# Performance work log

Measured on AMD Instinct MI355X. Metric: run time of the kernel, lower is better.

Reference implementation:

```python
import jax, jax.numpy as jnp
import numpy as np

# Dimensions (ModelNet40-style point-cloud classification)
B, N, KNN, T = 4, 1024, 20, 10
BETA, LAM, EPS = 1.0, 1.0, 1e-6
TAU, TH_POS, TH_NEG = 20.0, 1.0, -1.0
NUM_CLASSES = 40


@jax.custom_vjp
def spike(x):
    # Heaviside with fast-sigmoid surrogate gradient (standard SNN practice)
    return (x >= 0).astype(x.dtype)

def _spike_fwd(x):
    return (x >= 0).astype(x.dtype), x

def _spike_bwd(x, g):
    return (g / (1.0 + jnp.abs(x)) ** 2,)

spike.defvjp(_spike_fwd, _spike_bwd)


def setup_inputs() -> dict:
    key = jax.random.key(0)
    ks = jax.random.split(key, 8)

    def lin(k, fin, fout):
        return jax.random.normal(k, (fin, fout), jnp.float32) / float(np.sqrt(fin))

    def cheb(k, fin, fout):  # [K=3, F_in, F_out] Chebyshev filter bank
        return jax.random.normal(k, (3, fin, fout), jnp.float32) / float(np.sqrt(fin))

    return {
        "point_cloud": jax.random.normal(ks[0], (B, N, 3), jnp.float32),
        "enc_W": lin(ks[1], 3, 64), "enc_b": jnp.zeros((64,), jnp.float32),
        "W0": cheb(ks[2], 64, 64), "b0": jnp.zeros((64,), jnp.float32),
        "W1": cheb(ks[3], 128, 128), "b1": jnp.zeros((128,), jnp.float32),
        "W2": cheb(ks[4], 256, 256), "b2": jnp.zeros((256,), jnp.float32),
        "ro_W": lin(ks[5], 512, NUM_CLASSES), "ro_b": jnp.zeros((NUM_CLASSES,), jnp.float32),
    }


def build_graph(pc):
    # Local-density-adaptive kNN graph: [B,N,KNN] neighbor idx, edge weights, per-node scale
    d2 = jnp.sum((pc[:, :, None, :] - pc[:, None, :, :]) ** 2, -1)  # [B,N,N]
    d2 = d2 + jnp.eye(pc.shape[1], dtype=pc.dtype) * 1e9            # exclude self
    negv, idx = jax.lax.top_k(-d2, KNN)
    dist = jnp.sqrt(jnp.maximum(-negv, 1e-12))                      # [B,N,KNN]
    sigma = BETA * jnp.mean(dist, -1) + EPS                         # adaptive sigma [B,N]
    w = jnp.exp(-dist ** 2 / sigma[..., None] ** 2)
    w = w / (jnp.sum(w, -1, keepdims=True) + EPS)                   # row-normalized
    return idx, w, LAM * sigma                                      # s_local = lambda*sigma


def lap_apply(x, idx, w, s):
    # Node-adaptive scaled Laplacian: s_i * (x_i - sum_j w_ij x_j); x: [B,T,N,F]
    neigh = jax.vmap(lambda xb, ib: xb[:, ib])(x, idx)              # [B,T,N,KNN,F]
    agg = jnp.einsum('bnk,btnkf->btnf', w, neigh)
    return s[:, None, :, None] * (x - agg)


def wavelet_conv(x, idx, w, s, Wc, bc):
    # Chebyshev order-3 graph wavelet conv: T0=x, T1=Lx, T2=2L(T1)-T0
    t1 = lap_apply(x, idx, w, s)
    t2 = 2.0 * lap_apply(t1, idx, w, s) - x
    return jnp.einsum('kbtnf,kfg->btng', jnp.stack([x, t1, t2]), Wc) + bc


def bipolar_lif(x):
    # Bipolar LIF with dual thresholds; soft reset; output concat([pos, neg]) doubles F
    decay = jnp.exp(jnp.asarray(-1.0 / TAU, x.dtype))
    def step(v, xt):
        v = decay * v + xt
        sp = spike(v - TH_POS)
        sn = spike(TH_NEG - v)
        v = v - sp * TH_POS - sn * TH_NEG
        return v, jnp.concatenate([sp, sn], -1)
    v0 = jnp.zeros((x.shape[0],) + x.shape[2:], x.dtype)
    _, out = jax.lax.scan(step, v0, jnp.swapaxes(x, 0, 1))          # scan over T
    return jnp.swapaxes(out, 0, 1)                                  # [B,T,N,2F]


def reference(point_cloud, enc_W, enc_b, W0, b0, W1, b1, W2, b2, ro_W, ro_b):
    idx, w, s = build_graph(point_cloud)
    feat = jax.nn.relu(point_cloud @ enc_W + enc_b)                 # [B,N,64]
    rates = jnp.clip(feat, 0.0, 1.0)
    u = jax.random.uniform(jax.random.key(42), (feat.shape[0], T) + feat.shape[1:], feat.dtype)
    spikes = (u < rates[:, None]).astype(feat.dtype)                # Poisson rate encoding [B,T,N,64]
    for Wc, bc in ((W0, b0), (W1, b1), (W2, b2)):
        spikes = bipolar_lif(wavelet_conv(spikes, idx, w, s, Wc, bc))
    rate = jnp.mean(spikes, axis=1)                                 # rate readout over time
    pooled = jnp.mean(rate, axis=1)                                 # global average pool over nodes
    return pooled @ ro_W + ro_b                                     # [B, NUM_CLASSES]
```

## Files before the change

### kernel.cpp

```cpp
#include <hip/hip_runtime.h>
#include <stdint.h>
#include <math.h>

#pragma clang fp contract(off)

#define NB 4
#define NN 1024
#define KNN 20
#define NT 10

__global__ __launch_bounds__(256) void graph_kernel(const float* __restrict__ pc,
        int* __restrict__ idx_out, float* __restrict__ w_out, float* __restrict__ s_out){
  int row = blockIdx.x;
  int b = row >> 10, i = row & (NN-1);
  int tid = threadIdx.x;
  __shared__ float d2s[NN];
  __shared__ unsigned long long red[256];
  __shared__ int   sel_idx[KNN];
  __shared__ float sel_d2[KNN];
  const float* pb = pc + (size_t)b*NN*3;
  float xi = pb[i*3+0], yi = pb[i*3+1], zi = pb[i*3+2];
  for (int j=tid; j<NN; j+=256){
    float dx = xi - pb[j*3+0];
    float dy = yi - pb[j*3+1];
    float dz = zi - pb[j*3+2];
    float d2 = dx*dx;
    d2 = d2 + dy*dy;
    d2 = d2 + dz*dz;
    if (j==i) d2 = d2 + 1e9f;
    d2s[j] = d2;
  }
  __syncthreads();
  for (int k=0;k<KNN;k++){
    unsigned long long best = 0xffffffffffffffffull;
    for (int j=tid;j<NN;j+=256){
      unsigned long long key = ((unsigned long long)__float_as_uint(d2s[j])<<32) | (unsigned int)j;
      if (key < best) best = key;
    }
    red[tid] = best;
    __syncthreads();
    for (int off=128; off>0; off>>=1){
      if (tid < off){ if (red[tid+off] < red[tid]) red[tid] = red[tid+off]; }
      __syncthreads();
    }
    if (tid==0){
      unsigned long long bk = red[0];
      int bj = (int)(bk & 0xffffffffu);
      sel_idx[k] = bj;
      sel_d2[k]  = __uint_as_float((unsigned int)(bk >> 32));
      d2s[bj] = __uint_as_float(0x7f800000u);
    }
    __syncthreads();
  }
  if (tid==0){
    float dist[KNN]; float dsum = 0.0f;
    for (int k=0;k<KNN;k++){ dist[k] = sqrtf(fmaxf(sel_d2[k], 1e-12f)); dsum = dsum + dist[k]; }
    float sigma = dsum / 20.0f;
    sigma = 1.0f * sigma + 1e-6f;
    float s2 = sigma * sigma;
    float wv[KNN]; float wsum = 0.0f;
    for (int k=0;k<KNN;k++){
      float ds = dist[k]*dist[k];
      wv[k] = expf((-ds)/s2);
      wsum = wsum + wv[k];
    }
    float denom = wsum + 1e-6f;
    for (int k=0;k<KNN;k++){
      w_out[(size_t)row*KNN+k]  = wv[k] / denom;
      idx_out[(size_t)row*KNN+k] = sel_idx[k];
    }
    s_out[row] = 1.0f * sigma;
  }
}

__global__ void enc_kernel(const float* __restrict__ pc, const float* __restrict__ W,
                           const float* __restrict__ bias, float* __restrict__ rates){
  int id = blockIdx.x*blockDim.x + threadIdx.x;
  if (id >= NB*NN*64) return;
  int f = id & 63; int bn = id >> 6;
  float p0 = pc[bn*3+0], p1 = pc[bn*3+1], p2 = pc[bn*3+2];
  float acc = fmaf(p0, W[0*64+f], 0.0f);
  acc = fmaf(p1, W[1*64+f], acc);
  acc = fmaf(p2, W[2*64+f], acc);
  acc = acc + bias[f];
  acc = fmaxf(acc, 0.0f);
  acc = fminf(fmaxf(acc, 0.0f), 1.0f);
  rates[id] = acc;
}

__device__ __forceinline__ uint32_t rotl32(uint32_t x, uint32_t r){ return (x<<r) | (x>>(32u-r)); }

__global__ void poisson_kernel(const float* __restrict__ rates, uint8_t* __restrict__ out){
  const uint32_t H = (uint32_t)(NB*NT*NN*64) / 2u;
  uint32_t i = blockIdx.x*blockDim.x + threadIdx.x;
  if (i >= H) return;
  const uint32_t ks0 = 0u, ks1 = 42u;
  const uint32_t ks2 = ks0 ^ ks1 ^ 0x1BD11BDAu;
  uint32_t x0 = i + ks0;
  uint32_t x1 = (i + H) + ks1;
#define TF4(a,b,c,d) \
  x0 += x1; x1 = rotl32(x1,a); x1 ^= x0; \
  x0 += x1; x1 = rotl32(x1,b); x1 ^= x0; \
  x0 += x1; x1 = rotl32(x1,c); x1 ^= x0; \
  x0 += x1; x1 = rotl32(x1,d); x1 ^= x0;
  TF4(13u,15u,26u,6u)  x0 += ks1; x1 += ks2 + 1u;
  TF4(17u,29u,16u,24u) x0 += ks2; x1 += ks0 + 2u;
  TF4(13u,15u,26u,6u)  x0 += ks0; x1 += ks1 + 3u;
  TF4(17u,29u,16u,24u) x0 += ks1; x1 += ks2 + 4u;
  TF4(13u,15u,26u,6u)  x0 += ks2; x1 += ks0 + 5u;
#undef TF4
  {
    uint32_t m = i;
    float u = __uint_as_float((x0 >> 9) | 0x3f800000u) - 1.0f;
    uint32_t f = m & 63u, n = (m >> 6) & (NN-1);
    uint32_t bt = m >> 16; uint32_t b = bt / NT;
    float rate = rates[(((size_t)b<<10) + n)*64 + f];
    out[m] = (u < rate) ? (uint8_t)1 : (uint8_t)0;
  }
  {
    uint32_t m = i + H;
    float u = __uint_as_float((x1 >> 9) | 0x3f800000u) - 1.0f;
    uint32_t f = m & 63u, n = (m >> 6) & (NN-1);
    uint32_t bt = m >> 16; uint32_t b = bt / NT;
    float rate = rates[(((size_t)b<<10) + n)*64 + f];
    out[m] = (u < rate) ? (uint8_t)1 : (uint8_t)0;
  }
}

__global__ void lap1_all_kernel(const uint8_t* __restrict__ x, const int* __restrict__ idx,
        const float* __restrict__ w, const float* __restrict__ s,
        float* __restrict__ t1, int t0, int F){
  int blk = blockIdx.x; int f = threadIdx.x;
  int bn = blk % (NB*NN); int tt = blk / (NB*NN);
  int b = bn >> 10; int n = bn & (NN-1); int t = t0 + tt;
  __shared__ int nidx[KNN]; __shared__ float nw[KNN]; __shared__ float sv;
  if (f < KNN){ nidx[f] = idx[(size_t)bn*KNN+f]; nw[f] = w[(size_t)bn*KNN+f]; }
  if (f == 0) sv = s[bn];
  __syncthreads();
  const uint8_t* xb = x + ((size_t)(b*NT + t)*NN)*F;
  float acc = 0.0f;
  for (int k=0;k<KNN;k++)
    acc = fmaf(nw[k], (float)xb[(size_t)nidx[k]*F + f], acc);
  float xv = (float)xb[(size_t)n*F + f];
  t1[((size_t)tt*(NB*NN) + bn)*F + f] = sv * (xv - acc);
}

__global__ void lap2_all_kernel(const uint8_t* __restrict__ x, const float* __restrict__ t1,
        const int* __restrict__ idx, const float* __restrict__ w, const float* __restrict__ s,
        float* __restrict__ t2, int t0, int F){
  int blk = blockIdx.x; int f = threadIdx.x;
  int bn = blk % (NB*NN); int tt = blk / (NB*NN);
  int b = bn >> 10; int n = bn & (NN-1); int t = t0 + tt;
  __shared__ int nidx[KNN]; __shared__ float nw[KNN]; __shared__ float sv;
  if (f < KNN){ nidx[f] = idx[(size_t)bn*KNN+f]; nw[f] = w[(size_t)bn*KNN+f]; }
  if (f == 0) sv = s[bn];
  __syncthreads();
  const float* t1b = t1 + ((size_t)tt*(NB*NN) + (size_t)b*NN)*F;
  float acc = 0.0f;
  for (int k=0;k<KNN;k++)
    acc = fmaf(nw[k], t1b[(size_t)nidx[k]*F + f], acc);
  float tv = t1[((size_t)tt*(NB*NN) + bn)*F + f];
  float lapv = sv * (tv - acc);
  const uint8_t* xb = x + ((size_t)(b*NT + t)*NN)*F;
  float xv = (float)xb[(size_t)n*F + f];
  t2[((size_t)tt*(NB*NN) + bn)*F + f] = 2.0f * lapv - xv;
}

template<int F, int G, int BN, int TN>
__global__ __launch_bounds__(256) void conv_gemm_kernel(const uint8_t* __restrict__ x,
        const float* __restrict__ t1, const float* __restrict__ t2,
        const float* __restrict__ W, float* __restrict__ abuf, int t0){
  constexpr int BM = 64, BK = 16, TM = 4;
  constexpr int NTX = BN / TN;
  constexpr int LDA = BM + 4;
  constexpr int LDB = BN + 4;
  __shared__ float As[BK * LDA];
  __shared__ float Ws[BK * LDB];

  const int tid = threadIdx.x;
  const int tx = tid % NTX, ty = tid / NTX;
  const int row0 = blockIdx.x * BM;
  const int g0 = blockIdx.y * BN;

  const int arow = tid >> 2;
  const int akg  = (tid & 3) * 4;
  const int grow = row0 + arow;
  const int tt_a = grow / (NB*NN);
  const int bn_a = grow % (NB*NN);
  const int b_a = bn_a >> 10, n_a = bn_a & (NN-1);
  const uint8_t* xrow  = x  + ((size_t)(b_a*NT + t0 + tt_a)*NN + n_a)*F;
  const float*   t1row = t1 + (size_t)grow * F;
  const float*   t2row = t2 + (size_t)grow * F;

  float acc[TM][TN];
  #pragma unroll
  for (int r=0;r<TM;r++)
    #pragma unroll
    for (int c=0;c<TN;c++) acc[r][c] = 0.0f;

  for (int s = 0; s < 3; ++s){
    for (int f0 = 0; f0 < F; f0 += BK){
      if (s == 0){
        uchar4 u = *(const uchar4*)(xrow + f0 + akg);
        As[(akg+0)*LDA + arow] = (float)u.x;
        As[(akg+1)*LDA + arow] = (float)u.y;
        As[(akg+2)*LDA + arow] = (float)u.z;
        As[(akg+3)*LDA + arow] = (float)u.w;
      } else {
        const float* src = ((s==1) ? t1row : t2row) + f0 + akg;
        float4 v = *(const float4*)src;
        As[(akg+0)*LDA + arow] = v.x;
        As[(akg+1)*LDA + arow] = v.y;
        As[(akg+2)*LDA + arow] = v.z;
        As[(akg+3)*LDA + arow] = v.w;
      }
      const float* Wsrc = W + ((size_t)(s*F + f0))*G + g0;
      #pragma unroll
      for (int e = 0; e < (BK*BN)/(256*4); ++e){
        int idx = tid + e*256;
        int wk = idx / (BN/4);
        int wg = (idx % (BN/4))*4;
        *(float4*)&Ws[wk*LDB + wg] = *(const float4*)(Wsrc + (size_t)wk*G + wg);
      }
      __syncthreads();
      #pragma unroll
      for (int k = 0; k < BK; ++k){
        float a[TM];
        *(float4*)a = *(const float4*)&As[k*LDA + ty*TM];
        float wv[TN];
        #pragma unroll
        for (int c = 0; c < TN; c += 4)
          *(float4*)&wv[c] = *(const float4*)&Ws[k*LDB + tx*TN + c];
        #pragma unroll
        for (int r=0;r<TM;r++)
          #pragma unroll
          for (int c=0;c<TN;c++)
            acc[r][c] = fmaf(a[r], wv[c], acc[r][c]);
      }
      __syncthreads();
    }
  }
  #pragma unroll
  for (int r=0;r<TM;r++){
    float* dst = abuf + (size_t)(row0 + ty*TM + r)*G + g0 + tx*TN;
    #pragma unroll
    for (int c=0;c<TN;c+=4)
      *(float4*)(dst + c) = *(float4*)&acc[r][c];
  }
}

__global__ void lif_kernel(const float* __restrict__ abuf, const float* __restrict__ bias,
        float* __restrict__ vbuf, uint8_t* __restrict__ out, int t0, int tc, int G, float decay){
  int id = blockIdx.x*blockDim.x + threadIdx.x;
  if (id >= NB*NN*G) return;
  int g = id % G;
  int bn = id / G;
  int b = bn >> 10, n = bn & (NN-1);
  float v = (t0 == 0) ? 0.0f : vbuf[id];
  float bg = bias[g];
  for (int tt=0; tt<tc; ++tt){
    float a = abuf[((size_t)tt*(NB*NN) + bn)*G + g] + bg;
    float vn = decay * v + a;
    float sp  = ((vn - 1.0f) >= 0.0f) ? 1.0f : 0.0f;
    float snk = ((-1.0f - vn) >= 0.0f) ? 1.0f : 0.0f;
    vn = vn - sp * 1.0f;
    vn = vn - snk * (-1.0f);
    v = vn;
    uint8_t* ob = out + ((size_t)(b*NT + t0 + tt)*NN + n)*((size_t)2*G);
    ob[g]   = (uint8_t)sp;
    ob[G+g] = (uint8_t)snk;
  }
  if (t0 + tc < NT) vbuf[id] = v;
}

__global__ void pool_partial_kernel(const uint8_t* __restrict__ sp, uint32_t* __restrict__ partial){
  int b = blockIdx.x >> 6;
  int chunk = blockIdx.x & 63;
  int n0 = chunk * 16;
  int u = threadIdx.x;
  uint32_t c0=0,c1=0,c2=0,c3=0;
  for (int t=0;t<NT;t++){
    for (int n=0;n<16;n++){
      const uint32_t* rowp = (const uint32_t*)(sp + ((size_t)(b*NT+t)*NN + n0+n)*512);
      uint32_t wv = rowp[u];
      c0 += wv & 0xffu;
      c1 += (wv >> 8) & 0xffu;
      c2 += (wv >> 16) & 0xffu;
      c3 += wv >> 24;
    }
  }
  uint32_t* op = partial + (size_t)blockIdx.x*512 + u*4;
  op[0]=c0; op[1]=c1; op[2]=c2; op[3]=c3;
}

__global__ __launch_bounds__(512) void finalize_head_kernel(const uint32_t* __restrict__ partial,
        const float* __restrict__ roW, const float* __restrict__ rob, float* __restrict__ out){
  int b = blockIdx.x;
  int f = threadIdx.x;
  __shared__ float pooled[512];
  uint32_t cnt = 0;
  for (int ch=0; ch<64; ch++)
    cnt += partial[((size_t)(b*64+ch))*512 + f];
  pooled[f] = (float)cnt / 10.0f / 1024.0f;
  __syncthreads();
  if (f < 40){
    float acc = 0.0f;
    for (int k=0;k<512;k++)
      acc = fmaf(pooled[k], roW[k*40+f], acc);
    out[b*40 + f] = acc + rob[f];
  }
}

extern "C" void kernel_launch(void* const* d_in, const int* in_sizes, int n_in,
                              void* d_out, int out_size, void* d_ws, size_t ws_size,
                              hipStream_t stream) {
  const float* pc   = (const float*)d_in[0];
  const float* encW = (const float*)d_in[1];
  const float* encB = (const float*)d_in[2];
  const float* W0   = (const float*)d_in[3];
  const float* b0   = (const float*)d_in[4];
  const float* W1   = (const float*)d_in[5];
  const float* b1   = (const float*)d_in[6];
  const float* W2   = (const float*)d_in[7];
  const float* b2   = (const float*)d_in[8];
  const float* roW  = (const float*)d_in[9];
  const float* rob  = (const float*)d_in[10];
  float* outp = (float*)d_out;

  char* p = (char*)d_ws;
  auto alloc = [&](size_t bytes)->char*{
    char* r = p; p += (bytes + 255) & ~(size_t)255; return r;
  };
  int*      idxb   = (int*)     alloc((size_t)NB*NN*KNN*4);
  float*    wb     = (float*)   alloc((size_t)NB*NN*KNN*4);
  float*    sb     = (float*)   alloc((size_t)NB*NN*4);
  float*    rates  = (float*)   alloc((size_t)NB*NN*64*4);
  float*    vbuf   = (float*)   alloc((size_t)NB*NN*256*4);
  uint32_t* partial= (uint32_t*)alloc((size_t)NB*64*512*4);
  uint8_t*  bufA   = (uint8_t*) alloc((size_t)NB*NT*NN*512);
  uint8_t*  bufB   = (uint8_t*) alloc((size_t)NB*NT*NN*512);

  size_t used = (size_t)(p - (char*)d_ws);
  size_t per_t = (size_t)NB*NN*256*4*3;
  int TC = 1;
  if (ws_size > used + per_t){
    size_t tcc = (ws_size - used) / per_t;
    TC = (tcc >= NT) ? NT : (int)tcc;
    if (TC < 1) TC = 1;
  }
  float* t1b  = (float*)alloc((size_t)NB*(size_t)TC*NN*256*4);
  float* t2b  = (float*)alloc((size_t)NB*(size_t)TC*NN*256*4);
  float* abuf = (float*)alloc((size_t)NB*(size_t)TC*NN*256*4);

  graph_kernel<<<NB*NN, 256, 0, stream>>>(pc, idxb, wb, sb);
  enc_kernel<<<(NB*NN*64 + 255)/256, 256, 0, stream>>>(pc, encW, encB, rates);
  {
    const uint32_t H = (uint32_t)(NB*NT*NN*64) / 2u;
    poisson_kernel<<<(H + 255)/256, 256, 0, stream>>>(rates, bufA);
  }

  float decay = expf(-1.0f / 20.0f);

  uint8_t* xin  = bufA;
  uint8_t* xout = bufB;
  for (int l=0; l<3; l++){
    int F = (l==0)?64:(l==1)?128:256;
    int G = F;
    const float* Wc = (l==0)?W0:(l==1)?W1:W2;
    const float* bc = (l==0)?b0:(l==1)?b1:b2;
    for (int t0=0; t0<NT; t0+=TC){
      int tc = (NT - t0 < TC) ? (NT - t0) : TC;
      int M = NB*NN*tc;
      lap1_all_kernel<<<NB*NN*tc, F, 0, stream>>>(xin, idxb, wb, sb, t1b, t0, F);
      lap2_all_kernel<<<NB*NN*tc, F, 0, stream>>>(xin, t1b, idxb, wb, sb, t2b, t0, F);
      if (l==0){
        dim3 grid(M/64, 1);
        conv_gemm_kernel<64,64,64,4><<<grid, 256, 0, stream>>>(xin, t1b, t2b, Wc, abuf, t0);
      } else if (l==1){
        dim3 grid(M/64, 2);
        conv_gemm_kernel<128,128,64,4><<<grid, 256, 0, stream>>>(xin, t1b, t2b, Wc, abuf, t0);
      } else {
        dim3 grid(M/64, 2);
        conv_gemm_kernel<256,256,128,8><<<grid, 256, 0, stream>>>(xin, t1b, t2b, Wc, abuf, t0);
      }
      lif_kernel<<<(NB*NN*G + 255)/256, 256, 0, stream>>>(abuf, bc, vbuf, xout, t0, tc, G, decay);
    }
    uint8_t* tmp = xin; xin = xout; xout = tmp;
  }

  pool_partial_kernel<<<NB*64, 128, 0, stream>>>(xin, partial);
  finalize_head_kernel<<<NB, 512, 0, stream>>>(partial, roW, rob, outp);
}
```

Measured before the change: 549.3 us.

## Pack multiple rows per Laplacian block and enlarge GEMM tiles to 128 rows

The Laplacian kernels are templated on F and now process 256/F rows per 256-thread block, so the small 64- and 128-wide layers no longer launch one tiny block per row. The conv GEMM tile grows from 64 to 128 rows with 8 rows per thread. Each thread's rows and columns are split into two halves to keep shared-memory reads conflict-free, and layer 1 now uses a single 128-wide column tile. This raises arithmetic intensity and per-thread reuse but increases register pressure and reduces the number of GEMM blocks.

```diff
diff --git a/kernel.cpp b/kernel.cpp
--- a/kernel.cpp
+++ b/kernel.cpp
@@ -127,51 +127,68 @@
   }
 }
 
-__global__ void lap1_all_kernel(const uint8_t* __restrict__ x, const int* __restrict__ idx,
-        const float* __restrict__ w, const float* __restrict__ s,
-        float* __restrict__ t1, int t0, int F){
-  int blk = blockIdx.x; int f = threadIdx.x;
-  int bn = blk % (NB*NN); int tt = blk / (NB*NN);
+template<int F>
+__global__ __launch_bounds__(256) void lap1_kernel2(const uint8_t* __restrict__ x,
+        const int* __restrict__ idx, const float* __restrict__ w, const float* __restrict__ s,
+        float* __restrict__ t1, int t0){
+  constexpr int R = 256 / F;
+  int tid = threadIdx.x;
+  int rsub = tid / F;
+  int f = tid % F;
+  int row = blockIdx.x * R + rsub;
+  int bn = row % (NB*NN); int tt = row / (NB*NN);
   int b = bn >> 10; int n = bn & (NN-1); int t = t0 + tt;
-  __shared__ int nidx[KNN]; __shared__ float nw[KNN]; __shared__ float sv;
-  if (f < KNN){ nidx[f] = idx[(size_t)bn*KNN+f]; nw[f] = w[(size_t)bn*KNN+f]; }
-  if (f == 0) sv = s[bn];
+  __shared__ int   nidx[R][KNN];
+  __shared__ float nw[R][KNN];
+  __shared__ float sv[R];
+  if (f < KNN){ nidx[rsub][f] = idx[(size_t)bn*KNN+f]; nw[rsub][f] = w[(size_t)bn*KNN+f]; }
+  if (f == 0) sv[rsub] = s[bn];
   __syncthreads();
   const uint8_t* xb = x + ((size_t)(b*NT + t)*NN)*F;
   float acc = 0.0f;
   for (int k=0;k<KNN;k++)
-    acc = fmaf(nw[k], (float)xb[(size_t)nidx[k]*F + f], acc);
+    acc = fmaf(nw[rsub][k], (float)xb[(size_t)nidx[rsub][k]*F + f], acc);
   float xv = (float)xb[(size_t)n*F + f];
-  t1[((size_t)tt*(NB*NN) + bn)*F + f] = sv * (xv - acc);
-}
-
-__global__ void lap2_all_kernel(const uint8_t* __restrict__ x, const float* __restrict__ t1,
-        const int* __restrict__ idx, const float* __restrict__ w, const float* __restrict__ s,
-        float* __restrict__ t2, int t0, int F){
-  int blk = blockIdx.x; int f = threadIdx.x;
-  int bn = blk % (NB*NN); int tt = blk / (NB*NN);
+  t1[(size_t)row*F + f] = sv[rsub] * (xv - acc);
+}
+
+template<int F>
+__global__ __launch_bounds__(256) void lap2_kernel2(const uint8_t* __restrict__ x,
+        const float* __restrict__ t1, const int* __restrict__ idx, const float* __restrict__ w,
+        const float* __restrict__ s, float* __restrict__ t2, int t0){
+  constexpr int R = 256 / F;
+  int tid = threadIdx.x;
+  int rsub = tid / F;
+  int f = tid % F;
+  int row = blockIdx.x * R + rsub;
+  int bn = row % (NB*NN); int tt = row / (NB*NN);
   int b = bn >> 10; int n = bn & (NN-1); int t = t0 + tt;
-  __shared__ int nidx[KNN]; __shared__ float nw[KNN]; __shared__ float sv;
-  if (f < KNN){ nidx[f] = idx[(size_t)bn*KNN+f]; nw[f] = w[(size_t)bn*KNN+f]; }
-  if (f == 0) sv = s[bn];
+  __shared__ int   nidx[R][KNN];
+  __shared__ float nw[R][KNN];
+  __shared__ float sv[R];
+  if (f < KNN){ nidx[rsub][f] = idx[(size_t)bn*KNN+f]; nw[rsub][f] = w[(size_t)bn*KNN+f]; }
+  if (f == 0) sv[rsub] = s[bn];
   __syncthreads();
   const float* t1b = t1 + ((size_t)tt*(NB*NN) + (size_t)b*NN)*F;
   float acc = 0.0f;
   for (int k=0;k<KNN;k++)
-    acc = fmaf(nw[k], t1b[(size_t)nidx[k]*F + f], acc);
-  float tv = t1[((size_t)tt*(NB*NN) + bn)*F + f];
-  float lapv = sv * (tv - acc);
+    acc = fmaf(nw[rsub][k], t1b[(size_t)nidx[rsub][k]*F + f], acc);
+  float tv = t1[(size_t)row*F + f];
+  float lapv = sv[rsub] * (tv - acc);
   const uint8_t* xb = x + ((size_t)(b*NT + t)*NN)*F;
   float xv = (float)xb[(size_t)n*F + f];
-  t2[((size_t)tt*(NB*NN) + bn)*F + f] = 2.0f * lapv - xv;
+  t2[(size_t)row*F + f] = 2.0f * lapv - xv;
 }
 
 template<int F, int G, int BN, int TN>
-__global__ __launch_bounds__(256) void conv_gemm_kernel(const uint8_t* __restrict__ x,
+__global__ __launch_bounds__(256) void conv_gemm2_kernel(const uint8_t* __restrict__ x,
         const float* __restrict__ t1, const float* __restrict__ t2,
         const float* __restrict__ W, float* __restrict__ abuf, int t0){
-  constexpr int BM = 64, BK = 16, TM = 4;
+  constexpr int BM = 128, BK = 16, TM = 8;
   constexpr int NTX = BN / TN;
+  constexpr int NTY = 256 / NTX;
+  static_assert(NTY * TM == BM, "tile mismatch");
+  constexpr int TNH = TN / 2;
   constexpr int LDA = BM + 4;
   constexpr int LDB = BN + 4;
   __shared__ float As[BK * LDA];
@@ -182,11 +199,11 @@
   const int row0 = blockIdx.x * BM;
   const int g0 = blockIdx.y * BN;
 
-  const int arow = tid >> 2;
-  const int akg  = (tid & 3) * 4;
+  const int arow = tid >> 1;
+  const int akg  = (tid & 1) * 8;
   const int grow = row0 + arow;
+  const int bn_a = grow % (NB*NN);
   const int tt_a = grow / (NB*NN);
-  const int bn_a = grow % (NB*NN);
   const int b_a = bn_a >> 10, n_a = bn_a & (NN-1);
   const uint8_t* xrow  = x  + ((size_t)(b_a*NT + t0 + tt_a)*NN + n_a)*F;
   const float*   t1row = t1 + (size_t)grow * F;
@@ -201,36 +218,51 @@
   for (int s = 0; s < 3; ++s){
     for (int f0 = 0; f0 < F; f0 += BK){
       if (s == 0){
-        uchar4 u = *(const uchar4*)(xrow + f0 + akg);
-        As[(akg+0)*LDA + arow] = (float)u.x;
-        As[(akg+1)*LDA + arow] = (float)u.y;
-        As[(akg+2)*LDA + arow] = (float)u.z;
-        As[(akg+3)*LDA + arow] = (float)u.w;
+        uchar4 u0 = *(const uchar4*)(xrow + f0 + akg);
+        uchar4 u1 = *(const uchar4*)(xrow + f0 + akg + 4);
+        As[(akg+0)*LDA + arow] = (float)u0.x;
+        As[(akg+1)*LDA + arow] = (float)u0.y;
+        As[(akg+2)*LDA + arow] = (float)u0.z;
+        As[(akg+3)*LDA + arow] = (float)u0.w;
+        As[(akg+4)*LDA + arow] = (float)u1.x;
+        As[(akg+5)*LDA + arow] = (float)u1.y;
+        As[(akg+6)*LDA + arow] = (float)u1.z;
+        As[(akg+7)*LDA + arow] = (float)u1.w;
       } else {
         const float* src = ((s==1) ? t1row : t2row) + f0 + akg;
-        float4 v = *(const float4*)src;
-        As[(akg+0)*LDA + arow] = v.x;
-        As[(akg+1)*LDA + arow] = v.y;
-        As[(akg+2)*LDA + arow] = v.z;
-        As[(akg+3)*LDA + arow] = v.w;
+        float4 v0 = *(const float4*)src;
+        float4 v1 = *(const float4*)(src + 4);
+        As[(akg+0)*LDA + arow] = v0.x;
+        As[(akg+1)*LDA + arow] = v0.y;
+        As[(akg+2)*LDA + arow] = v0.z;
+        As[(akg+3)*LDA + arow] = v0.w;
+        As[(akg+4)*LDA + arow] = v1.x;
+        As[(akg+5)*LDA + arow] = v1.y;
+        As[(akg+6)*LDA + arow] = v1.z;
+        As[(akg+7)*LDA + arow] = v1.w;
       }
       const float* Wsrc = W + ((size_t)(s*F + f0))*G + g0;
       #pragma unroll
       for (int e = 0; e < (BK*BN)/(256*4); ++e){
-        int idx = tid + e*256;
-        int wk = idx / (BN/4);
-        int wg = (idx % (BN/4))*4;
+        int idx2 = tid + e*256;
+        int wk = idx2 / (BN/4);
+        int wg = (idx2 % (BN/4))*4;
         *(float4*)&Ws[wk*LDB + wg] = *(const float4*)(Wsrc + (size_t)wk*G + wg);
       }
       __syncthreads();
       #pragma unroll
       for (int k = 0; k < BK; ++k){
         float a[TM];
-        *(float4*)a = *(const float4*)&As[k*LDA + ty*TM];
+        *(float4*)&a[0] = *(const float4*)&As[k*LDA + ty*4];
+        *(float4*)&a[4] = *(const float4*)&As[k*LDA + BM/2 + ty*4];
         float wv[TN];
-        #pragma unroll
-        for (int c = 0; c < TN; c += 4)
-          *(float4*)&wv[c] = *(const float4*)&Ws[k*LDB + tx*TN + c];
+        if constexpr (TN == 8){
+          *(float4*)&wv[0] = *(const float4*)&Ws[k*LDB + tx*4];
+          *(float4*)&wv[4] = *(const float4*)&Ws[k*LDB + BN/2 + tx*4];
+        } else {
+          *(float2*)&wv[0] = *(const float2*)&Ws[k*LDB + tx*2];
+          *(float2*)&wv[2] = *(const float2*)&Ws[k*LDB + BN/2 + tx*2];
+        }
         #pragma unroll
         for (int r=0;r<TM;r++)
           #pragma unroll
@@ -241,11 +273,18 @@
     }
   }
   #pragma unroll
-  for (int r=0;r<TM;r++){
-    float* dst = abuf + (size_t)(row0 + ty*TM + r)*G + g0 + tx*TN;
+  for (int rg=0; rg<2; ++rg){
     #pragma unroll
-    for (int c=0;c<TN;c+=4)
-      *(float4*)(dst + c) = *(float4*)&acc[r][c];
+    for (int r=0; r<TM/2; ++r){
+      float* dst = abuf + (size_t)(row0 + rg*(BM/2) + ty*(TM/2) + r)*G + g0;
+      if constexpr (TN == 8){
+        *(float4*)(dst + tx*4)        = *(float4*)&acc[rg*(TM/2)+r][0];
+        *(float4*)(dst + BN/2 + tx*4) = *(float4*)&acc[rg*(TM/2)+r][4];
+      } else {
+        *(float2*)(dst + tx*2)        = *(float2*)&acc[rg*(TM/2)+r][0];
+        *(float2*)(dst + BN/2 + tx*2) = *(float2*)&acc[rg*(TM/2)+r][2];
+      }
+    }
   }
 }
 
@@ -364,24 +403,27 @@
   uint8_t* xin  = bufA;
   uint8_t* xout = bufB;
   for (int l=0; l<3; l++){
-    int F = (l==0)?64:(l==1)?128:256;
-    int G = F;
+    int G = (l==0)?64:(l==1)?128:256;
     const float* Wc = (l==0)?W0:(l==1)?W1:W2;
     const float* bc = (l==0)?b0:(l==1)?b1:b2;
     for (int t0=0; t0<NT; t0+=TC){
       int tc = (NT - t0 < TC) ? (NT - t0) : TC;
       int M = NB*NN*tc;
-      lap1_all_kernel<<<NB*NN*tc, F, 0, stream>>>(xin, idxb, wb, sb, t1b, t0, F);
-      lap2_all_kernel<<<NB*NN*tc, F, 0, stream>>>(xin, t1b, idxb, wb, sb, t2b, t0, F);
       if (l==0){
-        dim3 grid(M/64, 1);
-        conv_gemm_kernel<64,64,64,4><<<grid, 256, 0, stream>>>(xin, t1b, t2b, Wc, abuf, t0);
+        lap1_kernel2<64><<<M/4, 256, 0, stream>>>(xin, idxb, wb, sb, t1b, t0);
+        lap2_kernel2<64><<<M/4, 256, 0, stream>>>(xin, t1b, idxb, wb, sb, t2b, t0);
+        dim3 grid(M/128, 1);
+        conv_gemm2_kernel<64,64,64,4><<<grid, 256, 0, stream>>>(xin, t1b, t2b, Wc, abuf, t0);
       } else if (l==1){
-        dim3 grid(M/64, 2);
-        conv_gemm_kernel<128,128,64,4><<<grid, 256, 0, stream>>>(xin, t1b, t2b, Wc, abuf, t0);
+        lap1_kernel2<128><<<M/2, 256, 0, stream>>>(xin, idxb, wb, sb, t1b, t0);
+        lap2_kernel2<128><<<M/2, 256, 0, stream>>>(xin, t1b, idxb, wb, sb, t2b, t0);
+        dim3 grid(M/128, 1);
+        conv_gemm2_kernel<128,128,128,8><<<grid, 256, 0, stream>>>(xin, t1b, t2b, Wc, abuf, t0);
       } else {
-        dim3 grid(M/64, 2);
-        conv_gemm_kernel<256,256,128,8><<<grid, 256, 0, stream>>>(xin, t1b, t2b, Wc, abuf, t0);
+        lap1_kernel2<256><<<M, 256, 0, stream>>>(xin, idxb, wb, sb, t1b, t0);
+        lap2_kernel2<256><<<M, 256, 0, stream>>>(xin, t1b, idxb, wb, sb, t2b, t0);
+        dim3 grid(M/128, 2);
+        conv_gemm2_kernel<256,256,128,8><<<grid, 256, 0, stream>>>(xin, t1b, t2b, Wc, abuf, t0);
       }
       lif_kernel<<<(NB*NN*G + 255)/256, 256, 0, stream>>>(abuf, bc, vbuf, xout, t0, tc, G, decay);
     }
```

New measurement: 586.6 us. +6.8%, slower.

## Vectorize Laplacian gathers over multiple nodes per block and de-conflict GEMM LDS reads

Applied to the files above, without the earlier changes.

The Laplacian kernels now process several nodes per 256-thread block, and each thread handles four features using uchar4/float4 gathers and stores instead of one feature per thread with one block per node. This is meant to cut launch and block overhead, keep wavefronts full for small F, and widen memory transactions. The GEMM now has each thread read split-half fragments of the A and W tiles and store output the same way, which is meant to reduce LDS bank conflicts. The cost is more complex indexing and extra shared-memory staging of neighbor lists.

```diff
diff --git a/kernel.cpp b/kernel.cpp
--- a/kernel.cpp
+++ b/kernel.cpp
@@ -127,51 +127,101 @@
   }
 }
 
-__global__ void lap1_all_kernel(const uint8_t* __restrict__ x, const int* __restrict__ idx,
-        const float* __restrict__ w, const float* __restrict__ s,
-        float* __restrict__ t1, int t0, int F){
-  int blk = blockIdx.x; int f = threadIdx.x;
-  int bn = blk % (NB*NN); int tt = blk / (NB*NN);
+template<int F>
+__global__ __launch_bounds__(256) void lap1_kernel3(const uint8_t* __restrict__ x,
+        const int* __restrict__ idx, const float* __restrict__ w, const float* __restrict__ s,
+        float* __restrict__ t1, int t0){
+  constexpr int TPN = F / 4;
+  constexpr int R   = 256 / TPN;
+  int tid = threadIdx.x;
+  int rsub = tid / TPN;
+  int f4 = tid % TPN;
+  int row = blockIdx.x * R + rsub;
+  int bn = row % (NB*NN); int tt = row / (NB*NN);
   int b = bn >> 10; int n = bn & (NN-1); int t = t0 + tt;
-  __shared__ int nidx[KNN]; __shared__ float nw[KNN]; __shared__ float sv;
-  if (f < KNN){ nidx[f] = idx[(size_t)bn*KNN+f]; nw[f] = w[(size_t)bn*KNN+f]; }
-  if (f == 0) sv = s[bn];
+  __shared__ int   nidx[R][KNN];
+  __shared__ float nw[R][KNN];
+  __shared__ float sv[R];
+  int bn0 = (blockIdx.x * R) % (NB*NN);
+  for (int e=tid; e<R*KNN; e+=256){
+    int r = e / KNN, k = e % KNN;
+    nidx[r][k] = idx[(size_t)(bn0+r)*KNN+k];
+    nw[r][k]   = w[(size_t)(bn0+r)*KNN+k];
+  }
+  for (int e=tid; e<R; e+=256) sv[e] = s[bn0+e];
   __syncthreads();
   const uint8_t* xb = x + ((size_t)(b*NT + t)*NN)*F;
-  float acc = 0.0f;
-  for (int k=0;k<KNN;k++)
-    acc = fmaf(nw[k], (float)xb[(size_t)nidx[k]*F + f], acc);
-  float xv = (float)xb[(size_t)n*F + f];
-  t1[((size_t)tt*(NB*NN) + bn)*F + f] = sv * (xv - acc);
-}
-
-__global__ void lap2_all_kernel(const uint8_t* __restrict__ x, const float* __restrict__ t1,
-        const int* __restrict__ idx, const float* __restrict__ w, const float* __restrict__ s,
-        float* __restrict__ t2, int t0, int F){
-  int blk = blockIdx.x; int f = threadIdx.x;
-  int bn = blk % (NB*NN); int tt = blk / (NB*NN);
+  float a0=0.f,a1=0.f,a2=0.f,a3=0.f;
+  for (int k=0;k<KNN;k++){
+    float wk = nw[rsub][k];
+    uchar4 u = *(const uchar4*)(xb + (size_t)nidx[rsub][k]*F + f4*4);
+    a0 = fmaf(wk, (float)u.x, a0);
+    a1 = fmaf(wk, (float)u.y, a1);
+    a2 = fmaf(wk, (float)u.z, a2);
+    a3 = fmaf(wk, (float)u.w, a3);
+  }
+  uchar4 ux = *(const uchar4*)(xb + (size_t)n*F + f4*4);
+  float sl = sv[rsub];
+  float4 o;
+  o.x = sl * ((float)ux.x - a0);
+  o.y = sl * ((float)ux.y - a1);
+  o.z = sl * ((float)ux.z - a2);
+  o.w = sl * ((float)ux.w - a3);
+  *(float4*)(t1 + (size_t)row*F + f4*4) = o;
+}
+
+template<int F>
+__global__ __launch_bounds__(256) void lap2_kernel3(const uint8_t* __restrict__ x,
+        const float* __restrict__ t1, const int* __restrict__ idx, const float* __restrict__ w,
+        const float* __restrict__ s, float* __restrict__ t2, int t0){
+  constexpr int TPN = F / 4;
+  constexpr int R   = 256 / TPN;
+  int tid = threadIdx.x;
+  int rsub = tid / TPN;
+  int f4 = tid % TPN;
+  int row = blockIdx.x * R + rsub;
+  int bn = row % (NB*NN); int tt = row / (NB*NN);
   int b = bn >> 10; int n = bn & (NN-1); int t = t0 + tt;
-  __shared__ int nidx[KNN]; __shared__ float nw[KNN]; __shared__ float sv;
-  if (f < KNN){ nidx[f] = idx[(size_t)bn*KNN+f]; nw[f] = w[(size_t)bn*KNN+f]; }
-  if (f == 0) sv = s[bn];
+  __shared__ int   nidx[R][KNN];
+  __shared__ float nw[R][KNN];
+  __shared__ float sv[R];
+  int bn0 = (blockIdx.x * R) % (NB*NN);
+  for (int e=tid; e<R*KNN; e+=256){
+    int r = e / KNN, k = e % KNN;
+    nidx[r][k] = idx[(size_t)(bn0+r)*KNN+k];
+    nw[r][k]   = w[(size_t)(bn0+r)*KNN+k];
+  }
+  for (int e=tid; e<R; e+=256) sv[e] = s[bn0+e];
   __syncthreads();
   const float* t1b = t1 + ((size_t)tt*(NB*NN) + (size_t)b*NN)*F;
-  float acc = 0.0f;
-  for (int k=0;k<KNN;k++)
-    acc = fmaf(nw[k], t1b[(size_t)nidx[k]*F + f], acc);
-  float tv = t1[((size_t)tt*(NB*NN) + bn)*F + f];
-  float lapv = sv * (tv - acc);
-  const uint8_t* xb = x + ((size_t)(b*NT + t)*NN)*F;
-  float xv = (float)xb[(size_t)n*F + f];
-  t2[((size_t)tt*(NB*NN) + bn)*F + f] = 2.0f * lapv - xv;
+  float a0=0.f,a1=0.f,a2=0.f,a3=0.f;
+  for (int k=0;k<KNN;k++){
+    float wk = nw[rsub][k];
+    float4 v = *(const float4*)(t1b + (size_t)nidx[rsub][k]*F + f4*4);
+    a0 = fmaf(wk, v.x, a0);
+    a1 = fmaf(wk, v.y, a1);
+    a2 = fmaf(wk, v.z, a2);
+    a3 = fmaf(wk, v.w, a3);
+  }
+  float4 tv = *(const float4*)(t1 + (size_t)row*F + f4*4);
+  uchar4 ux = *(const uchar4*)(x + ((size_t)(b*NT + t)*NN + n)*F + f4*4);
+  float sl = sv[rsub];
+  float4 o;
+  o.x = 2.0f * (sl * (tv.x - a0)) - (float)ux.x;
+  o.y = 2.0f * (sl * (tv.y - a1)) - (float)ux.y;
+  o.z = 2.0f * (sl * (tv.z - a2)) - (float)ux.z;
+  o.w = 2.0f * (sl * (tv.w - a3)) - (float)ux.w;
+  *(float4*)(t2 + (size_t)row*F + f4*4) = o;
 }
 
 template<int F, int G, int BN, int TN>
-__global__ __launch_bounds__(256) void conv_gemm_kernel(const uint8_t* __restrict__ x,
+__global__ __launch_bounds__(256) void conv_gemm3_kernel(const uint8_t* __restrict__ x,
         const float* __restrict__ t1, const float* __restrict__ t2,
         const float* __restrict__ W, float* __restrict__ abuf, int t0){
   constexpr int BM = 64, BK = 16, TM = 4;
   constexpr int NTX = BN / TN;
+  constexpr int NTY = 256 / NTX;
+  static_assert(NTY * TM == BM, "tile mismatch");
   constexpr int LDA = BM + 4;
   constexpr int LDB = BN + 4;
   __shared__ float As[BK * LDA];
@@ -185,8 +235,8 @@
   const int arow = tid >> 2;
   const int akg  = (tid & 3) * 4;
   const int grow = row0 + arow;
+  const int bn_a = grow % (NB*NN);
   const int tt_a = grow / (NB*NN);
-  const int bn_a = grow % (NB*NN);
   const int b_a = bn_a >> 10, n_a = bn_a & (NN-1);
   const uint8_t* xrow  = x  + ((size_t)(b_a*NT + t0 + tt_a)*NN + n_a)*F;
   const float*   t1row = t1 + (size_t)grow * F;
@@ -217,20 +267,25 @@
       const float* Wsrc = W + ((size_t)(s*F + f0))*G + g0;
       #pragma unroll
       for (int e = 0; e < (BK*BN)/(256*4); ++e){
-        int idx = tid + e*256;
-        int wk = idx / (BN/4);
-        int wg = (idx % (BN/4))*4;
+        int idx2 = tid + e*256;
+        int wk = idx2 / (BN/4);
+        int wg = (idx2 % (BN/4))*4;
         *(float4*)&Ws[wk*LDB + wg] = *(const float4*)(Wsrc + (size_t)wk*G + wg);
       }
       __syncthreads();
       #pragma unroll
       for (int k = 0; k < BK; ++k){
         float a[TM];
-        *(float4*)a = *(const float4*)&As[k*LDA + ty*TM];
+        *(float2*)&a[0] = *(const float2*)&As[k*LDA + ty*2];
+        *(float2*)&a[2] = *(const float2*)&As[k*LDA + BM/2 + ty*2];
         float wv[TN];
-        #pragma unroll
-        for (int c = 0; c < TN; c += 4)
-          *(float4*)&wv[c] = *(const float4*)&Ws[k*LDB + tx*TN + c];
+        if constexpr (TN == 8){
+          *(float4*)&wv[0] = *(const float4*)&Ws[k*LDB + tx*4];
+          *(float4*)&wv[4] = *(const float4*)&Ws[k*LDB + BN/2 + tx*4];
+        } else {
+          *(float2*)&wv[0] = *(const float2*)&Ws[k*LDB + tx*2];
+          *(float2*)&wv[2] = *(const float2*)&Ws[k*LDB + BN/2 + tx*2];
+        }
         #pragma unroll
         for (int r=0;r<TM;r++)
           #pragma unroll
@@ -241,11 +296,18 @@
     }
   }
   #pragma unroll
-  for (int r=0;r<TM;r++){
-    float* dst = abuf + (size_t)(row0 + ty*TM + r)*G + g0 + tx*TN;
+  for (int rg=0; rg<2; ++rg){
     #pragma unroll
-    for (int c=0;c<TN;c+=4)
-      *(float4*)(dst + c) = *(float4*)&acc[r][c];
+    for (int r=0; r<TM/2; ++r){
+      float* dst = abuf + (size_t)(row0 + rg*(BM/2) + ty*2 + r)*G + g0;
+      if constexpr (TN == 8){
+        *(float4*)(dst + tx*4)        = *(float4*)&acc[rg*2+r][0];
+        *(float4*)(dst + BN/2 + tx*4) = *(float4*)&acc[rg*2+r][4];
+      } else {
+        *(float2*)(dst + tx*2)        = *(float2*)&acc[rg*2+r][0];
+        *(float2*)(dst + BN/2 + tx*2) = *(float2*)&acc[rg*2+r][2];
+      }
+    }
   }
 }
 
@@ -364,24 +426,27 @@
   uint8_t* xin  = bufA;
   uint8_t* xout = bufB;
   for (int l=0; l<3; l++){
-    int F = (l==0)?64:(l==1)?128:256;
-    int G = F;
+    int G = (l==0)?64:(l==1)?128:256;
     const float* Wc = (l==0)?W0:(l==1)?W1:W2;
     const float* bc = (l==0)?b0:(l==1)?b1:b2;
     for (int t0=0; t0<NT; t0+=TC){
       int tc = (NT - t0 < TC) ? (NT - t0) : TC;
       int M = NB*NN*tc;
-      lap1_all_kernel<<<NB*NN*tc, F, 0, stream>>>(xin, idxb, wb, sb, t1b, t0, F);
-      lap2_all_kernel<<<NB*NN*tc, F, 0, stream>>>(xin, t1b, idxb, wb, sb, t2b, t0, F);
       if (l==0){
+        lap1_kernel3<64><<<M/16, 256, 0, stream>>>(xin, idxb, wb, sb, t1b, t0);
+        lap2_kernel3<64><<<M/16, 256, 0, stream>>>(xin, t1b, idxb, wb, sb, t2b, t0);
         dim3 grid(M/64, 1);
-        conv_gemm_kernel<64,64,64,4><<<grid, 256, 0, stream>>>(xin, t1b, t2b, Wc, abuf, t0);
+        conv_gemm3_kernel<64,64,64,4><<<grid, 256, 0, stream>>>(xin, t1b, t2b, Wc, abuf, t0);
       } else if (l==1){
+        lap1_kernel3<128><<<M/8, 256, 0, stream>>>(xin, idxb, wb, sb, t1b, t0);
+        lap2_kernel3<128><<<M/8, 256, 0, stream>>>(xin, t1b, idxb, wb, sb, t2b, t0);
         dim3 grid(M/64, 2);
-        conv_gemm_kernel<128,128,64,4><<<grid, 256, 0, stream>>>(xin, t1b, t2b, Wc, abuf, t0);
+        conv_gemm3_kernel<128,128,64,4><<<grid, 256, 0, stream>>>(xin, t1b, t2b, Wc, abuf, t0);
       } else {
+        lap1_kernel3<256><<<M/4, 256, 0, stream>>>(xin, idxb, wb, sb, t1b, t0);
+        lap2_kernel3<256><<<M/4, 256, 0, stream>>>(xin, t1b, idxb, wb, sb, t2b, t0);
         dim3 grid(M/64, 2);
-        conv_gemm_kernel<256,256,128,8><<<grid, 256, 0, stream>>>(xin, t1b, t2b, Wc, abuf, t0);
+        conv_gemm3_kernel<256,256,128,8><<<grid, 256, 0, stream>>>(xin, t1b, t2b, Wc, abuf, t0);
       }
       lif_kernel<<<(NB*NN*G + 255)/256, 256, 0, stream>>>(abuf, bc, vbuf, xout, t0, tc, G, decay);
     }
```

New measurement: 532.1 us. 1.03x faster.
